# Performance work log

Hardware: AMD Instinct MI355X
Metric: run time of the kernel (lower is better)

Reference implementation:

```python
import jax, jax.numpy as jnp
import numpy as np

B, T, L = 256, 1024, 64
INIT = 0.1


def setup_inputs() -> dict:
    key = jax.random.key(0)
    k1, k2, k3, k4, k5 = jax.random.split(key, 5)
    scores = jax.random.normal(k1, (B, T, L), dtype=jnp.float32)
    targets = jax.random.randint(k2, (B, T), 0, L)
    start = jax.random.uniform(k3, (L,), dtype=jnp.float32, minval=-INIT, maxval=INIT)
    T_mat = jax.random.uniform(k4, (L, L), dtype=jnp.float32, minval=-INIT, maxval=INIT)
    end = jax.random.uniform(k5, (L,), dtype=jnp.float32, minval=-INIT, maxval=INIT)
    return {"scores": scores, "targets": targets, "start": start, "T_mat": T_mat, "end": end}


def reference(scores, targets, start, T_mat, end):
    # scores: [B,T,L], targets: [B,T] int, start/end: [L], T_mat: [L,L] with T_mat[cur, prev]
    Ttr = T_mat.T  # [prev, cur]

    # --- normalizers via forward algorithm (scan over time) ---
    prev0 = start[None, :] + scores[:, 0]  # [B,L]

    def step(prev, emit):  # prev [B,L], emit [B,L]
        cur = prev[:, :, None] + emit[:, None, :] + Ttr[None, :, :]  # [B,prev,cur]
        return jax.scipy.special.logsumexp(cur, axis=1), None

    emits_t = jnp.swapaxes(scores, 0, 1)[1:]  # [T-1,B,L]
    prev, _ = jax.lax.scan(step, prev0, emits_t)
    normalizers = jax.scipy.special.logsumexp(prev + end[None, :], axis=1)  # [B]

    # --- gold path score ---
    emits = jnp.take_along_axis(scores, targets[:, :, None], axis=2).squeeze(2).sum(axis=1)  # [B]
    trans = (start[targets[:, 0]]
             + T_mat[targets[:, 1:], targets[:, :-1]].sum(axis=1)
             + end[targets[:, -1]])  # [B]
    target_scores = emits + trans

    return (normalizers - target_scores).mean()
```

## Files before the change

kernel.cpp:

```cpp
#include <hip/hip_runtime.h>

#define NB 256
#define NT 1024
#define NL 64

typedef __fp16 h2v __attribute__((ext_vector_type(2)));

__device__ __forceinline__ float rfl_f(float v) {
  return __builtin_bit_cast(float, __builtin_amdgcn_readfirstlane(__builtin_bit_cast(int, v)));
}

__device__ __forceinline__ float dpp_xor1(float v) {
  int i = __builtin_bit_cast(int, v);
  int r = __builtin_amdgcn_update_dpp(i, i, 0xB1, 0xF, 0xF, false);
  return __builtin_bit_cast(float, r);
}

#define DOT4(P, B)                                                            \
  s0 = __builtin_amdgcn_fdot2(__builtin_bit_cast(h2v, (P).x), Rh[(B) + 0], s0, false); \
  s1 = __builtin_amdgcn_fdot2(__builtin_bit_cast(h2v, (P).y), Rh[(B) + 1], s1, false); \
  s2 = __builtin_amdgcn_fdot2(__builtin_bit_cast(h2v, (P).z), Rh[(B) + 2], s2, false); \
  s3 = __builtin_amdgcn_fdot2(__builtin_bit_cast(h2v, (P).w), Rh[(B) + 3], s3, false);

#define CRF_STEP(EF)                                                          \
  do {                                                                        \
    float wn = dpp_xor1(w);                                                   \
    h2v pk = __builtin_amdgcn_cvt_pkrtz(w, wn);                               \
    lb[wslot] = __builtin_bit_cast(int, pk);                                  \
    int4 P0 = lbv[0], P1 = lbv[1], P2 = lbv[2], P3 = lbv[3];                  \
    int4 P4 = lbv[4], P5 = lbv[5], P6 = lbv[6], P7 = lbv[7];                  \
    int e5 = (P0.x >> 10) & 0x1f;                                             \
    float K = __builtin_bit_cast(float, (130 - e5) << 23);                    \
    float KE = K * (EF);                                                      \
    e2 += e5 - 3;                                                             \
    float s0 = 0.f, s1 = 0.f, s2 = 0.f, s3 = 0.f;                             \
    DOT4(P0, 0); DOT4(P1, 4); DOT4(P2, 8); DOT4(P3, 12);                      \
    DOT4(P4, 16); DOT4(P5, 20); DOT4(P6, 24); DOT4(P7, 28);                   \
    w = ((s0 + s1) + (s2 + s3)) * KE;                                         \
  } while (0)

#define AQ __ATOMIC_ACQUIRE
#define RL __ATOMIC_RELEASE
#define SCOPE __HIP_MEMORY_SCOPE_AGENT

__global__ __launch_bounds__(64) void fb_kernel(const float* __restrict__ scores,
                                                const int* __restrict__ targets,
                                                const float* __restrict__ start,
                                                const float* __restrict__ Tm,
                                                const float* __restrict__ endv,
                                                float* __restrict__ wsA,
                                                float* __restrict__ wsG,
                                                float* __restrict__ wsL,
                                                int* __restrict__ flagF,
                                                int* __restrict__ flagG,
                                                int* __restrict__ cnt,
                                                float* __restrict__ out) {
  const int lane = threadIdx.x;
  const int bb = blockIdx.x;

  if (bb >= 2 * NB) {
    const int b = bb - 2 * NB;
    const int* tg = targets + b * NT;
    const float* sc = scores + (size_t)b * NT * NL;
    float acc = 0.f;
    for (int t = lane; t < NT; t += 64) {
      int c = tg[t];
      acc += sc[t * NL + c];
      if (t > 0) acc += Tm[c * NL + tg[t - 1]];
    }
#pragma unroll
    for (int off = 32; off > 0; off >>= 1) acc += __shfl_xor(acc, off, 64);
    if (lane == 0) wsG[b] = acc + start[tg[0]] + endv[tg[NT - 1]];
    __threadfence();
    if (lane == 0) __hip_atomic_store(&flagG[b], 1, RL, SCOPE);
    return;
  }

  __shared__ int4 lbv_s[16];
  int* lb = (int*)lbv_s;
  const int4* lbv = lbv_s;
  const int wslot = (lane & 1) * 32 + (lane >> 1);

  const bool bwd = bb >= NB;
  const int b = bwd ? bb - NB : bb;
  const float* sc = scores + (size_t)b * NT * NL;
  const float LN2 = 0.69314718055994530942f;

  const float* Tb = bwd ? (Tm + lane) : (Tm + lane * NL);
  const int str = bwd ? NL : 1;
  h2v Rh[32];
#pragma unroll
  for (int k = 0; k < 32; k++)
    Rh[k] = __builtin_amdgcn_cvt_pkrtz(__expf(Tb[(2 * k) * str]),
                                       __expf(Tb[(2 * k + 1) * str]));

  if (!bwd) {
    float a0 = start[lane] + sc[lane];
    float m0 = rfl_f(a0);
    float w = __expf(a0 - m0) * 16.f;
    int e2 = -4;

    float buf[4];
#pragma unroll
    for (int k = 0; k < 4; k++) buf[k] = sc[(1 + k) * NL + lane];

    for (int i = 0; i < 128; i++) {
      float nb4[4];
      int tb = 5 + 4 * i;
#pragma unroll
      for (int k = 0; k < 4; k++) nb4[k] = sc[(tb + k) * NL + lane];
      float Ev[4];
#pragma unroll
      for (int k = 0; k < 4; k++) Ev[k] = __expf(buf[k]);
      CRF_STEP(Ev[0]);
      CRF_STEP(Ev[1]);
      CRF_STEP(Ev[2]);
      CRF_STEP(Ev[3]);
#pragma unroll
      for (int k = 0; k < 4; k++) buf[k] = nb4[k];
    }
    wsA[b * NL + lane] = m0 + (float)e2 * LN2 + __logf(w);
    __threadfence();
    if (lane == 0) __hip_atomic_store(&flagF[b], 1, RL, SCOPE);
  } else {
    float a0 = endv[lane] + sc[(NT - 1) * NL + lane];
    float m0 = rfl_f(a0);
    float w = __expf(a0 - m0) * 16.f;
    int e2 = -4;

    float buf[4];
#pragma unroll
    for (int k = 0; k < 4; k++) buf[k] = sc[(1022 - k) * NL + lane];

    for (int i = 0; i < 127; i++) {
      float nb4[4];
      int tb = 1018 - 4 * i;
#pragma unroll
      for (int k = 0; k < 4; k++) nb4[k] = sc[(tb - k) * NL + lane];
      float Ev[4];
#pragma unroll
      for (int k = 0; k < 4; k++) Ev[k] = __expf(buf[k]);
      CRF_STEP(Ev[0]);
      CRF_STEP(Ev[1]);
      CRF_STEP(Ev[2]);
      CRF_STEP(Ev[3]);
#pragma unroll
      for (int k = 0; k < 4; k++) buf[k] = nb4[k];
    }
    CRF_STEP(__expf(sc[514 * NL + lane]));
    CRF_STEP(__expf(sc[513 * NL + lane]));
    CRF_STEP(1.0f);
    float bv = m0 + (float)e2 * LN2 + __logf(w);

    while (__hip_atomic_load(&flagF[b], AQ, SCOPE) == 0) __builtin_amdgcn_s_sleep(2);
    float v = wsA[b * NL + lane] + bv;
    float m = v;
#pragma unroll
    for (int off = 32; off > 0; off >>= 1) m = fmaxf(m, __shfl_xor(m, off, 64));
    float s = __expf(v - m);
#pragma unroll
    for (int off = 32; off > 0; off >>= 1) s += __shfl_xor(s, off, 64);
    while (__hip_atomic_load(&flagG[b], AQ, SCOPE) == 0) __builtin_amdgcn_s_sleep(2);
    float loss = (m + __logf(s)) - wsG[b];

    int old = -1;
    if (lane == 0) {
      wsL[b] = loss;
      __threadfence();
      old = __hip_atomic_fetch_add(cnt, 1, __ATOMIC_ACQ_REL, SCOPE);
    }
    old = __shfl(old, 0, 64);
    if (old == NB - 1) {
      __threadfence();
      float t0 = __builtin_bit_cast(float, __hip_atomic_load((int*)&wsL[lane], AQ, SCOPE));
      float t1 = __builtin_bit_cast(float, __hip_atomic_load((int*)&wsL[lane + 64], AQ, SCOPE));
      float t2 = __builtin_bit_cast(float, __hip_atomic_load((int*)&wsL[lane + 128], AQ, SCOPE));
      float t3 = __builtin_bit_cast(float, __hip_atomic_load((int*)&wsL[lane + 192], AQ, SCOPE));
      float tot = (t0 + t1) + (t2 + t3);
#pragma unroll
      for (int off = 32; off > 0; off >>= 1) tot += __shfl_xor(tot, off, 64);
      if (lane == 0) out[0] = tot * (1.0f / NB);
    }
  }
}

extern "C" void kernel_launch(void* const* d_in, const int* in_sizes, int n_in,
                              void* d_out, int out_size, void* d_ws, size_t ws_size,
                              hipStream_t stream) {
  const float* scores = (const float*)d_in[0];
  const int* targets = (const int*)d_in[1];
  const float* start = (const float*)d_in[2];
  const float* Tm = (const float*)d_in[3];
  const float* endv = (const float*)d_in[4];
  float* out = (float*)d_out;

  int* flagF = (int*)d_ws;
  int* flagG = flagF + NB;
  int* cnt = flagG + NB;
  float* wsG = (float*)(cnt + 64);
  float* wsL = wsG + NB;
  float* wsA = wsL + NB;

  hipMemsetAsync(flagF, 0, (2 * NB + 64) * sizeof(int), stream);
  fb_kernel<<<3 * NB, 64, 0, stream>>>(scores, targets, start, Tm, endv,
                                       wsA, wsG, wsL, flagF, flagG, cnt, out);
}
```

Baseline: 202.5 us.

## Fuse forward, backward and gold-path work into one wave per batch

Each batch element now runs in a single 64-lane block that interleaves the forward and backward recurrences step by step, with two independent dependency chains sharing LDS. The gold-path score is computed in the same block instead of a separate one, and the final mean is done by block 0 polling per-batch flags rather than through an atomic counter. This drops the launch from 768 to 256 blocks and removes the cross-block waits for forward and gold results, hiding latency through instruction-level parallelism instead. In exchange each wave holds twice the transition registers and runs its two chains serially, and block 0 spin-waits on every other block, which relies on all 256 blocks being resident at once.

```diff
diff --git a/kernel.cpp b/kernel.cpp
--- a/kernel.cpp
+++ b/kernel.cpp
@@ -16,171 +16,189 @@
   return __builtin_bit_cast(float, r);
 }
 
-#define DOT4(P, B)                                                            \
-  s0 = __builtin_amdgcn_fdot2(__builtin_bit_cast(h2v, (P).x), Rh[(B) + 0], s0, false); \
-  s1 = __builtin_amdgcn_fdot2(__builtin_bit_cast(h2v, (P).y), Rh[(B) + 1], s1, false); \
-  s2 = __builtin_amdgcn_fdot2(__builtin_bit_cast(h2v, (P).z), Rh[(B) + 2], s2, false); \
-  s3 = __builtin_amdgcn_fdot2(__builtin_bit_cast(h2v, (P).w), Rh[(B) + 3], s3, false);
-
-#define CRF_STEP(EF)                                                          \
+#define DOT4F(P, B)                                                           \
+  s0 = __builtin_amdgcn_fdot2(__builtin_bit_cast(h2v, (P).x), RhF[(B) + 0], s0, false); \
+  s1 = __builtin_amdgcn_fdot2(__builtin_bit_cast(h2v, (P).y), RhF[(B) + 1], s1, false); \
+  s2 = __builtin_amdgcn_fdot2(__builtin_bit_cast(h2v, (P).z), RhF[(B) + 2], s2, false); \
+  s3 = __builtin_amdgcn_fdot2(__builtin_bit_cast(h2v, (P).w), RhF[(B) + 3], s3, false);
+
+#define DOT4B(P, B)                                                           \
+  s0 = __builtin_amdgcn_fdot2(__builtin_bit_cast(h2v, (P).x), RhB[(B) + 0], s0, false); \
+  s1 = __builtin_amdgcn_fdot2(__builtin_bit_cast(h2v, (P).y), RhB[(B) + 1], s1, false); \
+  s2 = __builtin_amdgcn_fdot2(__builtin_bit_cast(h2v, (P).z), RhB[(B) + 2], s2, false); \
+  s3 = __builtin_amdgcn_fdot2(__builtin_bit_cast(h2v, (P).w), RhB[(B) + 3], s3, false);
+
+#define STEP2(EFF, EFB)                                                       \
   do {                                                                        \
-    float wn = dpp_xor1(w);                                                   \
-    h2v pk = __builtin_amdgcn_cvt_pkrtz(w, wn);                               \
-    lb[wslot] = __builtin_bit_cast(int, pk);                                  \
-    int4 P0 = lbv[0], P1 = lbv[1], P2 = lbv[2], P3 = lbv[3];                  \
-    int4 P4 = lbv[4], P5 = lbv[5], P6 = lbv[6], P7 = lbv[7];                  \
-    int e5 = (P0.x >> 10) & 0x1f;                                             \
-    float K = __builtin_bit_cast(float, (130 - e5) << 23);                    \
-    float KE = K * (EF);                                                      \
-    e2 += e5 - 3;                                                             \
+    float wnF = dpp_xor1(wF);                                                 \
+    float wnB = dpp_xor1(wB);                                                 \
+    h2v pkF = __builtin_amdgcn_cvt_pkrtz(wF, wnF);                            \
+    h2v pkB = __builtin_amdgcn_cvt_pkrtz(wB, wnB);                            \
+    lb[wslotF] = __builtin_bit_cast(int, pkF);                                \
+    lb[wslotB] = __builtin_bit_cast(int, pkB);                                \
+    int4 QF0 = lbvF[0], QF1 = lbvF[1], QF2 = lbvF[2], QF3 = lbvF[3];          \
+    int4 QF4 = lbvF[4], QF5 = lbvF[5], QF6 = lbvF[6], QF7 = lbvF[7];          \
+    int4 QB0 = lbvB[0], QB1 = lbvB[1], QB2 = lbvB[2], QB3 = lbvB[3];          \
+    int4 QB4 = lbvB[4], QB5 = lbvB[5], QB6 = lbvB[6], QB7 = lbvB[7];          \
+    int e5F = (QF0.x >> 10) & 0x1f;                                           \
+    int e5B = (QB0.x >> 10) & 0x1f;                                           \
+    float KEF = __builtin_bit_cast(float, (130 - e5F) << 23) * (EFF);         \
+    float KEB = __builtin_bit_cast(float, (130 - e5B) << 23) * (EFB);         \
+    e2F += e5F - 3;                                                           \
+    e2B += e5B - 3;                                                           \
+    {                                                                         \
+      float s0 = 0.f, s1 = 0.f, s2 = 0.f, s3 = 0.f;                           \
+      DOT4F(QF0, 0); DOT4F(QF1, 4); DOT4F(QF2, 8); DOT4F(QF3, 12);            \
+      DOT4F(QF4, 16); DOT4F(QF5, 20); DOT4F(QF6, 24); DOT4F(QF7, 28);         \
+      wF = ((s0 + s1) + (s2 + s3)) * KEF;                                     \
+    }                                                                         \
+    {                                                                         \
+      float s0 = 0.f, s1 = 0.f, s2 = 0.f, s3 = 0.f;                           \
+      DOT4B(QB0, 0); DOT4B(QB1, 4); DOT4B(QB2, 8); DOT4B(QB3, 12);            \
+      DOT4B(QB4, 16); DOT4B(QB5, 20); DOT4B(QB6, 24); DOT4B(QB7, 28);         \
+      wB = ((s0 + s1) + (s2 + s3)) * KEB;                                     \
+    }                                                                         \
+  } while (0)
+
+#define STEPF(EFF)                                                            \
+  do {                                                                        \
+    float wnF = dpp_xor1(wF);                                                 \
+    h2v pkF = __builtin_amdgcn_cvt_pkrtz(wF, wnF);                            \
+    lb[wslotF] = __builtin_bit_cast(int, pkF);                                \
+    int4 QF0 = lbvF[0], QF1 = lbvF[1], QF2 = lbvF[2], QF3 = lbvF[3];          \
+    int4 QF4 = lbvF[4], QF5 = lbvF[5], QF6 = lbvF[6], QF7 = lbvF[7];          \
+    int e5F = (QF0.x >> 10) & 0x1f;                                           \
+    float KEF = __builtin_bit_cast(float, (130 - e5F) << 23) * (EFF);         \
+    e2F += e5F - 3;                                                           \
     float s0 = 0.f, s1 = 0.f, s2 = 0.f, s3 = 0.f;                             \
-    DOT4(P0, 0); DOT4(P1, 4); DOT4(P2, 8); DOT4(P3, 12);                      \
-    DOT4(P4, 16); DOT4(P5, 20); DOT4(P6, 24); DOT4(P7, 28);                   \
-    w = ((s0 + s1) + (s2 + s3)) * KE;                                         \
+    DOT4F(QF0, 0); DOT4F(QF1, 4); DOT4F(QF2, 8); DOT4F(QF3, 12);              \
+    DOT4F(QF4, 16); DOT4F(QF5, 20); DOT4F(QF6, 24); DOT4F(QF7, 28);           \
+    wF = ((s0 + s1) + (s2 + s3)) * KEF;                                       \
   } while (0)
 
 #define AQ __ATOMIC_ACQUIRE
 #define RL __ATOMIC_RELEASE
 #define SCOPE __HIP_MEMORY_SCOPE_AGENT
 
-__global__ __launch_bounds__(64) void fb_kernel(const float* __restrict__ scores,
-                                                const int* __restrict__ targets,
-                                                const float* __restrict__ start,
-                                                const float* __restrict__ Tm,
-                                                const float* __restrict__ endv,
-                                                float* __restrict__ wsA,
-                                                float* __restrict__ wsG,
-                                                float* __restrict__ wsL,
-                                                int* __restrict__ flagF,
-                                                int* __restrict__ flagG,
-                                                int* __restrict__ cnt,
-                                                float* __restrict__ out) {
+__global__ __launch_bounds__(64)
+__attribute__((amdgpu_waves_per_eu(1, 1)))
+void fb_kernel(const float* __restrict__ scores,
+               const int* __restrict__ targets,
+               const float* __restrict__ start,
+               const float* __restrict__ Tm,
+               const float* __restrict__ endv,
+               float* __restrict__ wsL,
+               int* __restrict__ flagL,
+               float* __restrict__ out) {
   const int lane = threadIdx.x;
-  const int bb = blockIdx.x;
-
-  if (bb >= 2 * NB) {
-    const int b = bb - 2 * NB;
-    const int* tg = targets + b * NT;
-    const float* sc = scores + (size_t)b * NT * NL;
-    float acc = 0.f;
-    for (int t = lane; t < NT; t += 64) {
-      int c = tg[t];
-      acc += sc[t * NL + c];
-      if (t > 0) acc += Tm[c * NL + tg[t - 1]];
-    }
-#pragma unroll
-    for (int off = 32; off > 0; off >>= 1) acc += __shfl_xor(acc, off, 64);
-    if (lane == 0) wsG[b] = acc + start[tg[0]] + endv[tg[NT - 1]];
-    __threadfence();
-    if (lane == 0) __hip_atomic_store(&flagG[b], 1, RL, SCOPE);
-    return;
-  }
-
-  __shared__ int4 lbv_s[16];
-  int* lb = (int*)lbv_s;
-  const int4* lbv = lbv_s;
-  const int wslot = (lane & 1) * 32 + (lane >> 1);
-
-  const bool bwd = bb >= NB;
-  const int b = bwd ? bb - NB : bb;
+  const int b = blockIdx.x;
   const float* sc = scores + (size_t)b * NT * NL;
   const float LN2 = 0.69314718055994530942f;
 
-  const float* Tb = bwd ? (Tm + lane) : (Tm + lane * NL);
-  const int str = bwd ? NL : 1;
-  h2v Rh[32];
-#pragma unroll
-  for (int k = 0; k < 32; k++)
-    Rh[k] = __builtin_amdgcn_cvt_pkrtz(__expf(Tb[(2 * k) * str]),
-                                       __expf(Tb[(2 * k + 1) * str]));
-
-  if (!bwd) {
-    float a0 = start[lane] + sc[lane];
-    float m0 = rfl_f(a0);
-    float w = __expf(a0 - m0) * 16.f;
-    int e2 = -4;
-
-    float buf[4];
-#pragma unroll
-    for (int k = 0; k < 4; k++) buf[k] = sc[(1 + k) * NL + lane];
-
-    for (int i = 0; i < 128; i++) {
-      float nb4[4];
-      int tb = 5 + 4 * i;
-#pragma unroll
-      for (int k = 0; k < 4; k++) nb4[k] = sc[(tb + k) * NL + lane];
-      float Ev[4];
-#pragma unroll
-      for (int k = 0; k < 4; k++) Ev[k] = __expf(buf[k]);
-      CRF_STEP(Ev[0]);
-      CRF_STEP(Ev[1]);
-      CRF_STEP(Ev[2]);
-      CRF_STEP(Ev[3]);
-#pragma unroll
-      for (int k = 0; k < 4; k++) buf[k] = nb4[k];
+  const int* tg = targets + b * NT;
+  float gacc = 0.f;
+#pragma unroll
+  for (int k = 0; k < 16; k++) {
+    int t = lane + 64 * k;
+    int c = tg[t];
+    gacc += sc[t * NL + c];
+    if (t > 0) gacc += Tm[c * NL + tg[t - 1]];
+  }
+#pragma unroll
+  for (int off = 32; off > 0; off >>= 1) gacc += __shfl_xor(gacc, off, 64);
+  const float gold = gacc + start[tg[0]] + endv[tg[NT - 1]];
+
+  __shared__ int4 lbv_s[32];
+  int* lb = (int*)lbv_s;
+  const int4* lbvF = lbv_s;
+  const int4* lbvB = lbv_s + 16;
+  const int wslot = (lane & 1) * 32 + (lane >> 1);
+  const int wslotF = wslot;
+  const int wslotB = 64 + wslot;
+
+  const float* TbF = Tm + lane * NL;
+  const float* TbB = Tm + lane;
+  h2v RhF[32], RhB[32];
+#pragma unroll
+  for (int k = 0; k < 32; k++) {
+    RhF[k] = __builtin_amdgcn_cvt_pkrtz(__expf(TbF[2 * k]), __expf(TbF[2 * k + 1]));
+    RhB[k] = __builtin_amdgcn_cvt_pkrtz(__expf(TbB[(2 * k) * NL]),
+                                        __expf(TbB[(2 * k + 1) * NL]));
+  }
+
+  float a0F = start[lane] + sc[lane];
+  float m0F = rfl_f(a0F);
+  float wF = __expf(a0F - m0F) * 16.f;
+  int e2F = -4;
+  float a0B = endv[lane] + sc[(NT - 1) * NL + lane];
+  float m0B = rfl_f(a0B);
+  float wB = __expf(a0B - m0B) * 16.f;
+  int e2B = -4;
+
+  float bF0 = sc[1 * NL + lane], bF1 = sc[2 * NL + lane];
+  float bF2 = sc[3 * NL + lane], bF3 = sc[4 * NL + lane];
+  float bB0 = sc[1022 * NL + lane], bB1 = sc[1021 * NL + lane];
+  float bB2 = sc[1020 * NL + lane], bB3 = sc[1019 * NL + lane];
+
+  for (int i = 0; i < 127; i++) {
+    int tf = 5 + 4 * i;
+    int tb = 1018 - 4 * i;
+    float nF0 = sc[(tf + 0) * NL + lane], nF1 = sc[(tf + 1) * NL + lane];
+    float nF2 = sc[(tf + 2) * NL + lane], nF3 = sc[(tf + 3) * NL + lane];
+    float nB0 = sc[(tb - 0) * NL + lane], nB1 = sc[(tb - 1) * NL + lane];
+    float nB2 = sc[(tb - 2) * NL + lane], nB3 = sc[(tb - 3) * NL + lane];
+    float EF0 = __expf(bF0), EF1 = __expf(bF1), EF2 = __expf(bF2), EF3 = __expf(bF3);
+    float EB0 = __expf(bB0), EB1 = __expf(bB1), EB2 = __expf(bB2), EB3 = __expf(bB3);
+    STEP2(EF0, EB0);
+    STEP2(EF1, EB1);
+    STEP2(EF2, EB2);
+    STEP2(EF3, EB3);
+    bF0 = nF0; bF1 = nF1; bF2 = nF2; bF3 = nF3;
+    bB0 = nB0; bB1 = nB1; bB2 = nB2; bB3 = nB3;
+  }
+  {
+    float EF0 = __expf(bF0), EF1 = __expf(bF1), EF2 = __expf(bF2), EF3 = __expf(bF3);
+    float EB0 = __expf(bB0), EB1 = __expf(bB1);
+    STEP2(EF0, EB0);
+    STEP2(EF1, EB1);
+    STEP2(EF2, 1.0f);
+    STEPF(EF3);
+  }
+
+  float vA = m0F + (float)e2F * LN2 + __logf(wF);
+  float vB = m0B + (float)e2B * LN2 + __logf(wB);
+  float v = vA + vB;
+  float m = v;
+#pragma unroll
+  for (int off = 32; off > 0; off >>= 1) m = fmaxf(m, __shfl_xor(m, off, 64));
+  float s = __expf(v - m);
+#pragma unroll
+  for (int off = 32; off > 0; off >>= 1) s += __shfl_xor(s, off, 64);
+  float loss = (m + __logf(s)) - gold;
+
+  if (lane == 0) {
+    wsL[b] = loss;
+    __threadfence();
+    __hip_atomic_store(&flagL[b], 1, RL, SCOPE);
+  }
+
+  if (b == 0) {
+    for (;;) {
+      int f0 = __hip_atomic_load(&flagL[lane], AQ, SCOPE);
+      int f1 = __hip_atomic_load(&flagL[lane + 64], AQ, SCOPE);
+      int f2 = __hip_atomic_load(&flagL[lane + 128], AQ, SCOPE);
+      int f3 = __hip_atomic_load(&flagL[lane + 192], AQ, SCOPE);
+      if (__all((f0 & f1 & f2 & f3) != 0)) break;
+      __builtin_amdgcn_s_sleep(8);
     }
-    wsA[b * NL + lane] = m0 + (float)e2 * LN2 + __logf(w);
-    __threadfence();
-    if (lane == 0) __hip_atomic_store(&flagF[b], 1, RL, SCOPE);
-  } else {
-    float a0 = endv[lane] + sc[(NT - 1) * NL + lane];
-    float m0 = rfl_f(a0);
-    float w = __expf(a0 - m0) * 16.f;
-    int e2 = -4;
-
-    float buf[4];
-#pragma unroll
-    for (int k = 0; k < 4; k++) buf[k] = sc[(1022 - k) * NL + lane];
-
-    for (int i = 0; i < 127; i++) {
-      float nb4[4];
-      int tb = 1018 - 4 * i;
-#pragma unroll
-      for (int k = 0; k < 4; k++) nb4[k] = sc[(tb - k) * NL + lane];
-      float Ev[4];
-#pragma unroll
-      for (int k = 0; k < 4; k++) Ev[k] = __expf(buf[k]);
-      CRF_STEP(Ev[0]);
-      CRF_STEP(Ev[1]);
-      CRF_STEP(Ev[2]);
-      CRF_STEP(Ev[3]);
-#pragma unroll
-      for (int k = 0; k < 4; k++) buf[k] = nb4[k];
-    }
-    CRF_STEP(__expf(sc[514 * NL + lane]));
-    CRF_STEP(__expf(sc[513 * NL + lane]));
-    CRF_STEP(1.0f);
-    float bv = m0 + (float)e2 * LN2 + __logf(w);
-
-    while (__hip_atomic_load(&flagF[b], AQ, SCOPE) == 0) __builtin_amdgcn_s_sleep(2);
-    float v = wsA[b * NL + lane] + bv;
-    float m = v;
-#pragma unroll
-    for (int off = 32; off > 0; off >>= 1) m = fmaxf(m, __shfl_xor(m, off, 64));
-    float s = __expf(v - m);
-#pragma unroll
-    for (int off = 32; off > 0; off >>= 1) s += __shfl_xor(s, off, 64);
-    while (__hip_atomic_load(&flagG[b], AQ, SCOPE) == 0) __builtin_amdgcn_s_sleep(2);
-    float loss = (m + __logf(s)) - wsG[b];
-
-    int old = -1;
-    if (lane == 0) {
-      wsL[b] = loss;
-      __threadfence();
-      old = __hip_atomic_fetch_add(cnt, 1, __ATOMIC_ACQ_REL, SCOPE);
-    }
-    old = __shfl(old, 0, 64);
-    if (old == NB - 1) {
-      __threadfence();
-      float t0 = __builtin_bit_cast(float, __hip_atomic_load((int*)&wsL[lane], AQ, SCOPE));
-      float t1 = __builtin_bit_cast(float, __hip_atomic_load((int*)&wsL[lane + 64], AQ, SCOPE));
-      float t2 = __builtin_bit_cast(float, __hip_atomic_load((int*)&wsL[lane + 128], AQ, SCOPE));
-      float t3 = __builtin_bit_cast(float, __hip_atomic_load((int*)&wsL[lane + 192], AQ, SCOPE));
-      float tot = (t0 + t1) + (t2 + t3);
-#pragma unroll
-      for (int off = 32; off > 0; off >>= 1) tot += __shfl_xor(tot, off, 64);
-      if (lane == 0) out[0] = tot * (1.0f / NB);
-    }
+    float t0 = __builtin_bit_cast(float, __hip_atomic_load((int*)&wsL[lane], AQ, SCOPE));
+    float t1 = __builtin_bit_cast(float, __hip_atomic_load((int*)&wsL[lane + 64], AQ, SCOPE));
+    float t2 = __builtin_bit_cast(float, __hip_atomic_load((int*)&wsL[lane + 128], AQ, SCOPE));
+    float t3 = __builtin_bit_cast(float, __hip_atomic_load((int*)&wsL[lane + 192], AQ, SCOPE));
+    float tot = (t0 + t1) + (t2 + t3);
+#pragma unroll
+    for (int off = 32; off > 0; off >>= 1) tot += __shfl_xor(tot, off, 64);
+    if (lane == 0) out[0] = tot * (1.0f / NB);
   }
 }
 
@@ -194,14 +212,9 @@
   const float* endv = (const float*)d_in[4];
   float* out = (float*)d_out;
 
-  int* flagF = (int*)d_ws;
-  int* flagG = flagF + NB;
-  int* cnt = flagG + NB;
-  float* wsG = (float*)(cnt + 64);
-  float* wsL = wsG + NB;
-  float* wsA = wsL + NB;
-
-  hipMemsetAsync(flagF, 0, (2 * NB + 64) * sizeof(int), stream);
-  fb_kernel<<<3 * NB, 64, 0, stream>>>(scores, targets, start, Tm, endv,
-                                       wsA, wsG, wsL, flagF, flagG, cnt, out);
-}
+  int* flagL = (int*)d_ws;
+  float* wsL = (float*)(flagL + NB);
+
+  hipMemsetAsync(flagL, 0, NB * sizeof(int), stream);
+  fb_kernel<<<NB, 64, 0, stream>>>(scores, targets, start, Tm, endv, wsL, flagL, out);
+}
```

New measurement: 233.5 us. +15.3%, slower.
